# Performance work log

Hardware: AMD Instinct MI355X
Metric: run time of the kernel (lower is better)

The kernel has to match this reference:

```python
import jax, jax.numpy as jnp
import numpy as np

N_POINTS = 1048576
FEATURES = 64
RES = 256


def setup_inputs() -> dict:
    key = jax.random.key(0)
    k1, k2, k3, k4 = jax.random.split(key, 4)
    x = jax.random.uniform(k1, (N_POINTS, 3), jnp.float32, -1.0, 1.0)
    plane_xy = jax.random.normal(k2, (1, FEATURES, RES, RES), jnp.float32)
    plane_xz = jax.random.normal(k3, (1, FEATURES, RES, RES), jnp.float32)
    plane_yz = jax.random.normal(k4, (1, FEATURES, RES, RES), jnp.float32)
    pose = jnp.zeros((1,), jnp.float32)
    person_id = 0
    return {"x": x, "plane_xy": plane_xy, "plane_xz": plane_xz,
            "plane_yz": plane_yz, "pose": pose, "person_id": person_id}


def _grid_sample_points(plane, uv):
    """Bilinear sample. plane: [1,C,IH,IW], uv: [N,2] in [-1,1]. Returns [N,C].
    Matches the hand-rolled torch grid_sample (align_corners=True semantics,
    corner indices clamped, weights computed from unclamped floor coords)."""
    C, IH, IW = plane.shape[1], plane.shape[2], plane.shape[3]
    ix = (uv[:, 0] + 1.0) * 0.5 * (IW - 1)
    iy = (uv[:, 1] + 1.0) * 0.5 * (IH - 1)
    fx0 = jnp.floor(ix)
    fy0 = jnp.floor(iy)
    # bilinear weights (differentiable w.r.t. ix, iy)
    w_nw = (fx0 + 1.0 - ix) * (fy0 + 1.0 - iy)
    w_ne = (ix - fx0) * (fy0 + 1.0 - iy)
    w_sw = (fx0 + 1.0 - ix) * (iy - fy0)
    w_se = (ix - fx0) * (iy - fy0)
    # clamped integer corner indices (non-differentiable, as in torch no_grad)
    x0 = jnp.clip(fx0, 0, IW - 1).astype(jnp.int32)
    x1 = jnp.clip(fx0 + 1.0, 0, IW - 1).astype(jnp.int32)
    y0 = jnp.clip(fy0, 0, IH - 1).astype(jnp.int32)
    y1 = jnp.clip(fy0 + 1.0, 0, IH - 1).astype(jnp.int32)
    pf = plane.reshape(C, IH * IW)  # [C, IH*IW]
    v_nw = pf[:, y0 * IW + x0]  # [C, N]
    v_ne = pf[:, y0 * IW + x1]
    v_sw = pf[:, y1 * IW + x0]
    v_se = pf[:, y1 * IW + x1]
    out = v_nw * w_nw + v_ne * w_ne + v_sw * w_sw + v_se * w_se  # [C, N]
    return out.T  # [N, C]


def reference(x, plane_xy, plane_xz, plane_yz, pose, person_id):
    # person_id selects the (single) person's planes; pose is unused upstream.
    feat_xy = _grid_sample_points(plane_xy, x[:, [0, 1]])
    feat_xz = _grid_sample_points(plane_xz, x[:, [0, 2]])
    feat_yz = _grid_sample_points(plane_yz, x[:, [1, 2]])
    feat = (feat_xy + feat_xz + feat_yz) / 3.0  # [N, FEATURES]
    return feat
```

## Files before the change

### kernel.cpp

```cpp
#include <hip/hip_runtime.h>

#define N_POINTS 1048576
#define FEAT 64
#define RES 256
#define PLANE_ELEMS (FEAT * RES * RES)

typedef unsigned short ushort_t;
typedef float v4f __attribute__((ext_vector_type(4)));

__device__ __forceinline__ ushort_t f2bf(float f) {
  unsigned u = __float_as_uint(f);
  unsigned r = u + 0x7FFFu + ((u >> 16) & 1u);
  return (ushort_t)(r >> 16);
}

__global__ __launch_bounds__(256) void transpose_bf16(
    const float* __restrict__ pxy, const float* __restrict__ pxz,
    const float* __restrict__ pyz, ushort_t* __restrict__ dst) {
  __shared__ ushort_t tile[64][72];
  const int plane = blockIdx.y;
  const float* src = (plane == 0) ? pxy : ((plane == 1) ? pxz : pyz);
  ushort_t* out = dst + (size_t)plane * PLANE_ELEMS;
  const int p0 = blockIdx.x * 64;
  const int tid = threadIdx.x;
#pragma unroll
  for (int k = 0; k < 4; ++k) {
    int c = (tid >> 4) + k * 16;
    int pp = (tid & 15) * 4;
    float4 v = *(const float4*)(src + (size_t)c * (RES * RES) + p0 + pp);
    tile[pp + 0][c] = f2bf(v.x);
    tile[pp + 1][c] = f2bf(v.y);
    tile[pp + 2][c] = f2bf(v.z);
    tile[pp + 3][c] = f2bf(v.w);
  }
  __syncthreads();
#pragma unroll
  for (int k = 0; k < 2; ++k) {
    int idx = k * 256 + tid;
    int pp = idx >> 3;
    int c8 = (idx & 7) * 8;
    uint4 v = *(const uint4*)&tile[pp][c8];
    *(uint4*)(out + (size_t)(p0 + pp) * FEAT + c8) = v;
  }
}

__device__ __forceinline__ void unpack_fma(uint4 v, float w, float* acc) {
  acc[0] = fmaf(__uint_as_float(v.x << 16), w, acc[0]);
  acc[1] = fmaf(__uint_as_float(v.x & 0xFFFF0000u), w, acc[1]);
  acc[2] = fmaf(__uint_as_float(v.y << 16), w, acc[2]);
  acc[3] = fmaf(__uint_as_float(v.y & 0xFFFF0000u), w, acc[3]);
  acc[4] = fmaf(__uint_as_float(v.z << 16), w, acc[4]);
  acc[5] = fmaf(__uint_as_float(v.z & 0xFFFF0000u), w, acc[5]);
  acc[6] = fmaf(__uint_as_float(v.w << 16), w, acc[6]);
  acc[7] = fmaf(__uint_as_float(v.w & 0xFFFF0000u), w, acc[7]);
}

__device__ __forceinline__ void sample_plane(const ushort_t* __restrict__ tp,
                                             float u, float v, int c8,
                                             float* acc) {
  float ix = (u + 1.0f) * 0.5f * (float)(RES - 1);
  float iy = (v + 1.0f) * 0.5f * (float)(RES - 1);
  float fx0 = floorf(ix), fy0 = floorf(iy);
  float wx1 = ix - fx0, wy1 = iy - fy0;
  float wx0 = fx0 + 1.0f - ix, wy0 = fy0 + 1.0f - iy;
  int x0 = min(max((int)fx0, 0), RES - 1);
  int y0 = min(max((int)fy0, 0), RES - 1);
  int x1 = min(max((int)fx0 + 1, 0), RES - 1);
  int y1 = min(max((int)fy0 + 1, 0), RES - 1);

  const uint4 v00 = *(const uint4*)(tp + (size_t)(y0 * RES + x0) * FEAT + c8);
  const uint4 v01 = *(const uint4*)(tp + (size_t)(y0 * RES + x1) * FEAT + c8);
  const uint4 v10 = *(const uint4*)(tp + (size_t)(y1 * RES + x0) * FEAT + c8);
  const uint4 v11 = *(const uint4*)(tp + (size_t)(y1 * RES + x1) * FEAT + c8);

  unpack_fma(v00, wx0 * wy0, acc);
  unpack_fma(v01, wx1 * wy0, acc);
  unpack_fma(v10, wx0 * wy1, acc);
  unpack_fma(v11, wx1 * wy1, acc);
}

__global__ __launch_bounds__(256) void triplane_sample_bf16(
    const float* __restrict__ x, const ushort_t* __restrict__ tps,
    float* __restrict__ out) {
  int t = blockIdx.x * 256 + threadIdx.x;
  int n = t >> 3;
  int c8 = (t & 7) << 3;

  float px = __builtin_nontemporal_load(x + n * 3 + 0);
  float py = __builtin_nontemporal_load(x + n * 3 + 1);
  float pz = __builtin_nontemporal_load(x + n * 3 + 2);

  float acc[8] = {0.f, 0.f, 0.f, 0.f, 0.f, 0.f, 0.f, 0.f};
  sample_plane(tps, px, py, c8, acc);
  sample_plane(tps + PLANE_ELEMS, px, pz, c8, acc);
  sample_plane(tps + 2 * PLANE_ELEMS, py, pz, c8, acc);

  const float s = 1.0f / 3.0f;
  v4f lo = {acc[0] * s, acc[1] * s, acc[2] * s, acc[3] * s};
  v4f hi = {acc[4] * s, acc[5] * s, acc[6] * s, acc[7] * s};
  float* o = out + (size_t)n * FEAT + c8;
  __builtin_nontemporal_store(lo, (v4f*)o);
  __builtin_nontemporal_store(hi, (v4f*)(o + 4));
}

__device__ __forceinline__ float sample_one(const float* __restrict__ pc,
                                            float u, float v) {
  float ix = (u + 1.0f) * 0.5f * (float)(RES - 1);
  float iy = (v + 1.0f) * 0.5f * (float)(RES - 1);
  float fx0 = floorf(ix), fy0 = floorf(iy);
  float wx1 = ix - fx0, wy1 = iy - fy0;
  float wx0 = fx0 + 1.0f - ix, wy0 = fy0 + 1.0f - iy;
  int x0 = min(max((int)fx0, 0), RES - 1);
  int y0 = min(max((int)fy0, 0), RES - 1);
  int x1 = min(max((int)fx0 + 1, 0), RES - 1);
  int y1 = min(max((int)fy0 + 1, 0), RES - 1);
  return pc[y0 * RES + x0] * (wx0 * wy0) + pc[y0 * RES + x1] * (wx1 * wy0) +
         pc[y1 * RES + x0] * (wx0 * wy1) + pc[y1 * RES + x1] * (wx1 * wy1);
}

__global__ __launch_bounds__(256) void triplane_direct(
    const float* __restrict__ x, const float* __restrict__ pxy,
    const float* __restrict__ pxz, const float* __restrict__ pyz,
    float* __restrict__ out) {
  int t = blockIdx.x * 256 + threadIdx.x;
  int n = t >> 6;
  int c = t & 63;
  float px = x[n * 3 + 0];
  float py = x[n * 3 + 1];
  float pz = x[n * 3 + 2];
  const size_t cs = (size_t)c * (RES * RES);
  float acc = sample_one(pxy + cs, px, py) + sample_one(pxz + cs, px, pz) +
              sample_one(pyz + cs, py, pz);
  out[(size_t)n * FEAT + c] = acc * (1.0f / 3.0f);
}

extern "C" void kernel_launch(void* const* d_in, const int* in_sizes, int n_in,
                              void* d_out, int out_size, void* d_ws,
                              size_t ws_size, hipStream_t stream) {
  const float* x   = (const float*)d_in[0];
  const float* pxy = (const float*)d_in[1];
  const float* pxz = (const float*)d_in[2];
  const float* pyz = (const float*)d_in[3];
  float* out = (float*)d_out;

  const size_t need = (size_t)3 * PLANE_ELEMS * sizeof(ushort_t);
  if (ws_size >= need) {
    ushort_t* tps = (ushort_t*)d_ws;
    dim3 tgrid(RES * RES / 64, 3);
    transpose_bf16<<<tgrid, 256, 0, stream>>>(pxy, pxz, pyz, tps);
    triplane_sample_bf16<<<(N_POINTS * 8) / 256, 256, 0, stream>>>(x, tps, out);
  } else {
    triplane_direct<<<(N_POINTS * 64) / 256, 256, 0, stream>>>(x, pxy, pxz,
                                                               pyz, out);
  }
}
```

Before: 503.3 us.

## Bucket-sort points by Morton cell before triplane sampling for cache locality

Adds a counting sort of the query points into 32^3 Morton-ordered spatial buckets (histogram, single-block scan, atomic scatter into a float4 buffer carrying the original index). The sampling kernel then processes points in sorted order with an XCD-aware block swizzle, so nearby points share plane texels in L2/MALL, and it scatters results back to their original rows. The goal is to cut random gather traffic on the 25 MB bf16 plane buffer, at the cost of four extra launches, atomics, and a scattered output write pattern.

```diff
diff --git a/kernel.cpp b/kernel.cpp
--- a/kernel.cpp
+++ b/kernel.cpp
@@ -4,6 +4,12 @@
 #define FEAT 64
 #define RES 256
 #define PLANE_ELEMS (FEAT * RES * RES)
+
+#define BUCKET_G 32
+#define NBUCKET (BUCKET_G * BUCKET_G * BUCKET_G)
+
+#define SAMPLE_BLOCKS (N_POINTS / 32)
+#define SAMPLE_CPX (SAMPLE_BLOCKS / 8)
 
 typedef unsigned short ushort_t;
 typedef float v4f __attribute__((ext_vector_type(4)));
@@ -42,6 +48,75 @@
     uint4 v = *(const uint4*)&tile[pp][c8];
     *(uint4*)(out + (size_t)(p0 + pp) * FEAT + c8) = v;
   }
+}
+
+__device__ __forceinline__ unsigned part1by2(unsigned v) {
+  v &= 0x3FFu;
+  v = (v | (v << 16)) & 0x030000FFu;
+  v = (v | (v << 8)) & 0x0300F00Fu;
+  v = (v | (v << 4)) & 0x030C30C3u;
+  v = (v | (v << 2)) & 0x09249249u;
+  return v;
+}
+
+__device__ __forceinline__ unsigned morton_bucket(float px, float py, float pz) {
+  int bx = (int)((px + 1.0f) * (0.5f * BUCKET_G));
+  int by = (int)((py + 1.0f) * (0.5f * BUCKET_G));
+  int bz = (int)((pz + 1.0f) * (0.5f * BUCKET_G));
+  bx = min(max(bx, 0), BUCKET_G - 1);
+  by = min(max(by, 0), BUCKET_G - 1);
+  bz = min(max(bz, 0), BUCKET_G - 1);
+  return part1by2((unsigned)bx) | (part1by2((unsigned)by) << 1) |
+         (part1by2((unsigned)bz) << 2);
+}
+
+__global__ __launch_bounds__(256) void zero_hist(unsigned* __restrict__ h) {
+  h[blockIdx.x * 256 + threadIdx.x] = 0u;
+}
+
+__global__ __launch_bounds__(256) void bucket_count(
+    const float* __restrict__ x, unsigned* __restrict__ hist) {
+  int n = blockIdx.x * 256 + threadIdx.x;
+  float px = x[n * 3 + 0];
+  float py = x[n * 3 + 1];
+  float pz = x[n * 3 + 2];
+  atomicAdd(&hist[morton_bucket(px, py, pz)], 1u);
+}
+
+__global__ __launch_bounds__(1024) void scan_hist(
+    const unsigned* __restrict__ hist, unsigned* __restrict__ cursor) {
+  __shared__ unsigned part[1024];
+  const int tid = threadIdx.x;
+  unsigned local[32];
+  unsigned s = 0;
+#pragma unroll
+  for (int i = 0; i < 32; ++i) {
+    local[i] = s;
+    s += hist[tid * 32 + i];
+  }
+  part[tid] = s;
+  __syncthreads();
+  for (int off = 1; off < 1024; off <<= 1) {
+    unsigned add = (tid >= off) ? part[tid - off] : 0u;
+    __syncthreads();
+    part[tid] += add;
+    __syncthreads();
+  }
+  unsigned base = (tid == 0) ? 0u : part[tid - 1];
+#pragma unroll
+  for (int i = 0; i < 32; ++i) cursor[tid * 32 + i] = base + local[i];
+}
+
+__global__ __launch_bounds__(256) void bucket_scatter(
+    const float* __restrict__ x, unsigned* __restrict__ cursor,
+    float4* __restrict__ xs) {
+  int n = blockIdx.x * 256 + threadIdx.x;
+  float px = x[n * 3 + 0];
+  float py = x[n * 3 + 1];
+  float pz = x[n * 3 + 2];
+  unsigned b = morton_bucket(px, py, pz);
+  unsigned pos = atomicAdd(&cursor[b], 1u);
+  xs[pos] = make_float4(px, py, pz, __uint_as_float((unsigned)n));
 }
 
 __device__ __forceinline__ void unpack_fma(uint4 v, float w, float* acc) {
@@ -79,22 +154,43 @@
   unpack_fma(v11, wx1 * wy1, acc);
 }
 
+__global__ __launch_bounds__(256) void triplane_sample_sorted(
+    const float4* __restrict__ xs, const ushort_t* __restrict__ tps,
+    float* __restrict__ out) {
+  int bid = blockIdx.x;
+  int swz = (bid & 7) * SAMPLE_CPX + (bid >> 3);
+  int p = swz * 32 + (threadIdx.x >> 3);
+  int c8 = (threadIdx.x & 7) << 3;
+
+  v4f pt = __builtin_nontemporal_load((const v4f*)xs + p);
+  unsigned n = __float_as_uint(pt.w);
+
+  float acc[8] = {0.f, 0.f, 0.f, 0.f, 0.f, 0.f, 0.f, 0.f};
+  sample_plane(tps, pt.x, pt.y, c8, acc);
+  sample_plane(tps + PLANE_ELEMS, pt.x, pt.z, c8, acc);
+  sample_plane(tps + 2 * PLANE_ELEMS, pt.y, pt.z, c8, acc);
+
+  const float s = 1.0f / 3.0f;
+  v4f lo = {acc[0] * s, acc[1] * s, acc[2] * s, acc[3] * s};
+  v4f hi = {acc[4] * s, acc[5] * s, acc[6] * s, acc[7] * s};
+  float* o = out + (size_t)n * FEAT + c8;
+  __builtin_nontemporal_store(lo, (v4f*)o);
+  __builtin_nontemporal_store(hi, (v4f*)(o + 4));
+}
+
 __global__ __launch_bounds__(256) void triplane_sample_bf16(
     const float* __restrict__ x, const ushort_t* __restrict__ tps,
     float* __restrict__ out) {
   int t = blockIdx.x * 256 + threadIdx.x;
   int n = t >> 3;
   int c8 = (t & 7) << 3;
-
   float px = __builtin_nontemporal_load(x + n * 3 + 0);
   float py = __builtin_nontemporal_load(x + n * 3 + 1);
   float pz = __builtin_nontemporal_load(x + n * 3 + 2);
-
   float acc[8] = {0.f, 0.f, 0.f, 0.f, 0.f, 0.f, 0.f, 0.f};
   sample_plane(tps, px, py, c8, acc);
   sample_plane(tps + PLANE_ELEMS, px, pz, c8, acc);
   sample_plane(tps + 2 * PLANE_ELEMS, py, pz, c8, acc);
-
   const float s = 1.0f / 3.0f;
   v4f lo = {acc[0] * s, acc[1] * s, acc[2] * s, acc[3] * s};
   v4f hi = {acc[4] * s, acc[5] * s, acc[6] * s, acc[7] * s};
@@ -143,8 +239,25 @@
   const float* pyz = (const float*)d_in[3];
   float* out = (float*)d_out;
 
-  const size_t need = (size_t)3 * PLANE_ELEMS * sizeof(ushort_t);
-  if (ws_size >= need) {
+  const size_t tps_bytes = (size_t)3 * PLANE_ELEMS * sizeof(ushort_t);
+  const size_t xs_bytes  = (size_t)N_POINTS * sizeof(float4);
+  const size_t cnt_bytes = (size_t)NBUCKET * sizeof(unsigned);
+  const size_t need_sorted = tps_bytes + xs_bytes + 2 * cnt_bytes;
+
+  if (ws_size >= need_sorted) {
+    ushort_t* tps    = (ushort_t*)d_ws;
+    float4* xs       = (float4*)((char*)d_ws + tps_bytes);
+    unsigned* cursor = (unsigned*)((char*)d_ws + tps_bytes + xs_bytes);
+    unsigned* hist   = cursor + NBUCKET;
+
+    dim3 tgrid(RES * RES / 64, 3);
+    transpose_bf16<<<tgrid, 256, 0, stream>>>(pxy, pxz, pyz, tps);
+    zero_hist<<<NBUCKET / 256, 256, 0, stream>>>(hist);
+    bucket_count<<<N_POINTS / 256, 256, 0, stream>>>(x, hist);
+    scan_hist<<<1, 1024, 0, stream>>>(hist, cursor);
+    bucket_scatter<<<N_POINTS / 256, 256, 0, stream>>>(x, cursor, xs);
+    triplane_sample_sorted<<<SAMPLE_BLOCKS, 256, 0, stream>>>(xs, tps, out);
+  } else if (ws_size >= tps_bytes) {
     ushort_t* tps = (ushort_t*)d_ws;
     dim3 tgrid(RES * RES / 64, 3);
     transpose_bf16<<<tgrid, 256, 0, stream>>>(pxy, pxz, pyz, tps);
```

New measurement: 481.3 us. 4.4% less time.
